# Kernel optimization log

Measured on AMD Instinct MI355X. Metric: run time of the kernel, lower is better.

Reference implementation:

```python
import jax, jax.numpy as jnp
import numpy as np
from jax import lax

B, L, N_NODES, N_SEQ = 256, 15360, 16, 64


def _lstm_layer(x, wih, whh, bih, bhh):
    # x: (B, T, I); torch gate order i, f, g, o
    H = whh.shape[1]
    b = bih + bhh
    def step(carry, xt):
        h, c = carry
        gates = xt @ wih.T + h @ whh.T + b
        i, f, g, o = jnp.split(gates, 4, axis=-1)
        c = jax.nn.sigmoid(f) * c + jax.nn.sigmoid(i) * jnp.tanh(g)
        h = jax.nn.sigmoid(o) * jnp.tanh(c)
        return (h, c), h
    h0 = jnp.zeros((x.shape[0], H), x.dtype)
    _, ys = lax.scan(step, (h0, h0), x.transpose(1, 0, 2))
    return ys.transpose(1, 0, 2)


def setup_inputs() -> dict:
    ks = iter(jax.random.split(jax.random.key(0), 64))
    def rn(shape, scale=1.0):
        return (jax.random.normal(next(ks), shape) * scale).astype(jnp.float32)
    d = {"x": rn((B, 1, L))}
    chs = [1, 16, 32, 64]
    for i in range(3):
        cin, cout = chs[i], chs[i + 1]
        s = 1.0 / np.sqrt(cin * 5)
        d[f"cw{i}"] = rn((cout, cin, 5), s)
        d[f"cb{i}"] = rn((cout,), s)
        d[f"bng{i}"] = jnp.ones((cout,), jnp.float32)
        d[f"bnb{i}"] = jnp.zeros((cout,), jnp.float32)
        d[f"bnm{i}"] = jnp.zeros((cout,), jnp.float32)
        d[f"bnv{i}"] = jnp.ones((cout,), jnp.float32)
    Hh = 64
    for l in range(2):
        s = 1.0 / np.sqrt(Hh)
        d[f"wih{l}"] = rn((4 * Hh, 64), s)
        d[f"whh{l}"] = rn((4 * Hh, Hh), s)
        d[f"bih{l}"] = rn((4 * Hh,), s)
        d[f"bhh{l}"] = rn((4 * Hh,), s)
    gin = [256, 64, 64]
    for l in range(3):
        s = 1.0 / np.sqrt(gin[l])
        d[f"gw{l}"] = rn((64, gin[l]), s)
        d[f"gb{l}"] = rn((64,), s)
    d["clw"] = rn((5, 64), 0.125)
    d["clb"] = rn((5,), 0.125)
    return d


def reference(x, cw0, cb0, bng0, bnb0, bnm0, bnv0, cw1, cb1, bng1, bnb1, bnm1, bnv1, cw2, cb2, bng2, bnb2, bnm2, bnv2, wih0, whh0, bih0, bhh0, wih1, whh1, bih1, bhh1, gw0, gb0, gw1, gb1, gw2, gb2, clw, clb):
    h = x
    # CNN: [Conv1d(k=5,p=2) -> BN(eval) -> ReLU -> MaxPool(2)] x 3
    for cw, cb, g, b, m, v in ((cw0, cb0, bng0, bnb0, bnm0, bnv0),
                               (cw1, cb1, bng1, bnb1, bnm1, bnv1),
                               (cw2, cb2, bng2, bnb2, bnm2, bnv2)):
        h = lax.conv_general_dilated(h, cw, (1,), [(2, 2)], dimension_numbers=("NCH", "OIH", "NCH")) + cb[None, :, None]
        h = g[None, :, None] * (h - m[None, :, None]) * lax.rsqrt(v[None, :, None] + 1e-5) + b[None, :, None]
        h = jax.nn.relu(h)
        Bq, Cq, Lq = h.shape
        h = h.reshape(Bq, Cq, Lq // 2, 2).max(-1)
    # AdaptiveAvgPool1d(64): length divisible by 64 -> exact mean bins
    Bq, Cq, Lq = h.shape
    h = h.reshape(Bq, Cq, N_SEQ, Lq // N_SEQ).mean(-1)
    h = h.transpose(0, 2, 1)  # (B, 64, 64) = (batch, seq, channels)
    # 2-layer LSTM (dropout is identity in eval)
    h = _lstm_layer(h, wih0, whh0, bih0, bhh0)
    h = _lstm_layer(h, wih1, whh1, bih1, bhh1)
    # Graph builder: Pearson-style correlation + value thresholding
    Hf = h.reshape(Bq, -1)
    fpn = Hf.shape[1] // N_NODES  # 256 features per node
    nf = Hf[:, :N_NODES * fpn].reshape(Bq, N_NODES, fpn)
    cen = nf - nf.mean(-1, keepdims=True)
    nrm = cen / (jnp.std(cen, axis=-1, ddof=1, keepdims=True) + 1e-8)
    C = jnp.einsum("bnf,bmf->bnm", nrm, nrm) / fpn  # (B, N, N)
    Cf = C.reshape(Bq, -1)
    k = min(max(1, int((100.0 - 25.0) / 100.0 * Cf.shape[1])), Cf.shape[1] - 1)
    thr = jnp.sort(Cf, axis=1)[:, k - 1]  # torch.kthvalue(k)
    eye = jnp.eye(N_NODES, dtype=C.dtype)
    adj = (C > thr[:, None, None]).astype(C.dtype) * (1.0 - eye)
    # GCN: x = ReLU(W (x + A x) + b), 3 layers, then max over nodes
    g = nf
    for gw, gb in ((gw0, gb0), (gw1, gb1), (gw2, gb2)):
        g = jax.nn.relu((g + jnp.einsum("bnm,bmf->bnf", adj, g)) @ gw.T + gb)
    emb = g.max(axis=1)
    return emb @ clw.T + clb
```

## Files before the change

kernel.cpp:

```cpp
#include <hip/hip_runtime.h>
#include <math.h>

typedef __attribute__((ext_vector_type(2))) float v2f;

__global__ __launch_bounds__(256) void prep_weights_kernel(
    const float* __restrict__ cw0, const float* __restrict__ cb0,
    const float* __restrict__ bng0, const float* __restrict__ bnb0,
    const float* __restrict__ bnm0, const float* __restrict__ bnv0,
    const float* __restrict__ cw1, const float* __restrict__ cb1,
    const float* __restrict__ bng1, const float* __restrict__ bnb1,
    const float* __restrict__ bnm1, const float* __restrict__ bnv1,
    const float* __restrict__ cw2, const float* __restrict__ cb2,
    const float* __restrict__ bng2, const float* __restrict__ bnb2,
    const float* __restrict__ bnm2, const float* __restrict__ bnv2,
    const float* __restrict__ wih0, const float* __restrict__ whh0,
    const float* __restrict__ wih1, const float* __restrict__ whh1,
    float* __restrict__ wt1, float* __restrict__ b1,
    float* __restrict__ wt2, float* __restrict__ b2,
    float* __restrict__ w0f, float* __restrict__ b0f,
    float* __restrict__ wih0c, float* __restrict__ whh0c,
    float* __restrict__ wih1c, float* __restrict__ whh1c)
{
    int g = blockIdx.x * 256 + threadIdx.x;
    const int GS = 64 * 256;
    for (int i = g; i < 2560; i += GS) {
        int co = i & 31, r = i >> 5, t = r % 5, ci = r / 5;
        float s = bng1[co] * rsqrtf(bnv1[co] + 1e-5f);
        wt1[i] = cw1[(co * 16 + ci) * 5 + t] * s;
    }
    if (g < 32) {
        float s = bng1[g] * rsqrtf(bnv1[g] + 1e-5f);
        b1[g] = (cb1[g] - bnm1[g]) * s + bnb1[g];
    }
    for (int i = g; i < 10240; i += GS) {
        int co = i & 63, r = i >> 6, t = r % 5, ci = r / 5;
        float s = bng2[co] * rsqrtf(bnv2[co] + 1e-5f);
        wt2[i] = cw2[(co * 32 + ci) * 5 + t] * s;
    }
    if (g < 64) {
        float s = bng2[g] * rsqrtf(bnv2[g] + 1e-5f);
        b2[g] = (cb2[g] - bnm2[g]) * s + bnb2[g];
    }
    if (g < 80) {
        int co = g / 5;
        float s = bng0[co] * rsqrtf(bnv0[co] + 1e-5f);
        w0f[g] = cw0[g] * s;
    }
    if (g < 16) {
        float s = bng0[g] * rsqrtf(bnv0[g] + 1e-5f);
        b0f[g] = (cb0[g] - bnm0[g]) * s + bnb0[g];
    }
    for (int i = g; i < 16384; i += GS) {
        int c = i & 3, r = (i >> 2) & 255, k4 = i >> 10;
        int src = r * 64 + k4 * 4 + c;
        wih0c[i] = wih0[src];
        whh0c[i] = whh0[src];
        wih1c[i] = wih1[src];
        whh1c[i] = whh1[src];
    }
}

__global__ __launch_bounds__(256) void convall_kernel(
    const float* __restrict__ x,
    const float* __restrict__ w0f, const float* __restrict__ b0f,
    const float* __restrict__ wt1, const float* __restrict__ b1,
    const float* __restrict__ wt2, const float* __restrict__ b2,
    const float* __restrict__ wih0c,
    const float* __restrict__ bih0, const float* __restrict__ bhh0,
    float* __restrict__ xg0g)
{
    __shared__ float U[8096];
    float* raw = &U[4064];
    int b = blockIdx.y, bx = blockIdx.x, tid = threadIdx.x;
    const float* xb = x + (size_t)b * 15360;
    {
        int base = 480 * bx - 14;
        for (int i = tid; i < 508; i += 256) {
            int g = base + i;
            raw[i] = (g >= 0 && g < 15360) ? xb[g] : 0.f;
        }
    }
    __syncthreads();
    {
        int ci0 = tid >> 4, sub = tid & 15;
        float w0 = w0f[ci0*5+0], w1 = w0f[ci0*5+1], w2 = w0f[ci0*5+2],
              w3 = w0f[ci0*5+3], w4 = w0f[ci0*5+4];
        float bb = b0f[ci0];
        int r0g = 240 * bx - 6;
        for (int p = sub; p < 252; p += 16) {
            int r = r0g + p;
            float v = 0.f;
            if (r >= 0 && r < 7680) {
                int i0 = 2 * p;
                float c0 = raw[i0],   c1 = raw[i0+1], c2 = raw[i0+2],
                      c3 = raw[i0+3], c4 = raw[i0+4], c5 = raw[i0+5];
                float s0 = fmaf(w0,c0, fmaf(w1,c1, fmaf(w2,c2, fmaf(w3,c3, w4*c4))));
                float s1 = fmaf(w0,c1, fmaf(w1,c2, fmaf(w2,c3, fmaf(w3,c4, w4*c5))));
                v = fmaxf(fmaxf(s0, s1) + bb, 0.f);
            }
            U[ci0 * 254 + p] = v;
        }
    }
    __syncthreads();
    {
        int cg = tid >> 7, jj = tid & 127;
        int cgu = __builtin_amdgcn_readfirstlane(cg);
        if (tid < 64) { int co = tid >> 1, c = 124 + (tid & 1); U[4064 + co * 126 + c] = 0.f; }
        if (jj < 124) {
            const float* wb = wt1 + cgu * 16;
            v2f a0[8], a1[8];
#pragma unroll
            for (int q = 0; q < 8; ++q) { a0[q] = (v2f){0.f,0.f}; a1[q] = (v2f){0.f,0.f}; }
#pragma unroll 4
            for (int ci = 0; ci < 16; ++ci) {
                const float2* xr = reinterpret_cast<const float2*>(&U[ci * 254]);
                float2 xA = xr[jj], xB = xr[jj + 1], xC = xr[jj + 2];
                float xv[6] = { xA.x, xA.y, xB.x, xB.y, xC.x, xC.y };
#pragma unroll
                for (int t = 0; t < 5; ++t) {
                    const v2f* wp2 = reinterpret_cast<const v2f*>(wb + (ci * 5 + t) * 32);
                    v2f va = { xv[t], xv[t] };
                    v2f vc = { xv[t + 1], xv[t + 1] };
#pragma unroll
                    for (int q2 = 0; q2 < 8; ++q2) {
                        v2f w = wp2[q2];
                        a0[q2] = __builtin_elementwise_fma(w, va, a0[q2]);
                        a1[q2] = __builtin_elementwise_fma(w, vc, a1[q2]);
                    }
                }
            }
            int q = 120 * bx - 2 + jj;
            bool ok = (q >= 0 && q < 3840);
#pragma unroll
            for (int q2 = 0; q2 < 8; ++q2) {
#pragma unroll
                for (int cpp = 0; cpp < 2; ++cpp) {
                    int qq = 2 * q2 + cpp;
                    int co = cgu * 16 + qq;
                    float val = 0.f;
                    if (ok) val = fmaxf(fmaxf(a0[q2][cpp], a1[q2][cpp]) + b1[co], 0.f);
                    U[4064 + co * 126 + jj] = val;
                }
            }
        }
    }
    __syncthreads();
    {
        int cg = tid >> 6, jj = tid & 63;
        int jje = (jj < 59) ? jj : 59;
        int cgu = __builtin_amdgcn_readfirstlane(cg);
        const float* wb = wt2 + cgu * 16;
        v2f a0[8], a1[8];
#pragma unroll
        for (int q = 0; q < 8; ++q) { a0[q] = (v2f){0.f,0.f}; a1[q] = (v2f){0.f,0.f}; }
#pragma unroll 4
        for (int ci = 0; ci < 32; ++ci) {
            const float2* xr = reinterpret_cast<const float2*>(&U[4064 + ci * 126]);
            float2 xA = xr[jje], xB = xr[jje + 1], xC = xr[jje + 2];
            float xv[6] = { xA.x, xA.y, xB.x, xB.y, xC.x, xC.y };
#pragma unroll
            for (int t = 0; t < 5; ++t) {
                const v2f* wp2 = reinterpret_cast<const v2f*>(wb + (ci * 5 + t) * 64);
                v2f va = { xv[t], xv[t] };
                v2f vc = { xv[t + 1], xv[t + 1] };
#pragma unroll
                for (int q2 = 0; q2 < 8; ++q2) {
                    v2f w = wp2[q2];
                    a0[q2] = __builtin_elementwise_fma(w, va, a0[q2]);
                    a1[q2] = __builtin_elementwise_fma(w, vc, a1[q2]);
                }
            }
        }
        __syncthreads();
        if (jj < 60) {
#pragma unroll
            for (int q2 = 0; q2 < 8; ++q2) {
#pragma unroll
                for (int cpp = 0; cpp < 2; ++cpp) {
                    int qq = 2 * q2 + cpp;
                    int co = cgu * 16 + qq;
                    float m = fmaxf(a0[q2][cpp], a1[q2][cpp]) + b2[co];
                    U[co * 61 + jj] = fmaxf(m, 0.f);
                }
            }
        }
    }
    __syncthreads();
    if (tid < 128) {
        int co = tid & 63, bin = tid >> 6;
        const float* r = U + co * 61 + bin * 30;
        float s = 0.f;
#pragma unroll
        for (int k = 0; k < 30; ++k) s += r[k];
        U[3904 + bin * 64 + co] = s * (1.f / 30.f);
    }
    __syncthreads();
    {
        int r = tid;
        float bias0 = bih0[r] + bhh0[r];
        float wr0[64];
#pragma unroll
        for (int k4 = 0; k4 < 16; ++k4) {
            float4 w4 = reinterpret_cast<const float4*>(wih0c)[k4 * 256 + r];
            wr0[k4*4+0] = w4.x; wr0[k4*4+1] = w4.y;
            wr0[k4*4+2] = w4.z; wr0[k4*4+3] = w4.w;
        }
#pragma unroll
        for (int bin = 0; bin < 2; ++bin) {
            float s0 = bias0, s1 = 0.f, s2 = 0.f, s3 = 0.f;
#pragma unroll
            for (int k4 = 0; k4 < 16; ++k4) {
                float4 xv4 = *reinterpret_cast<const float4*>(&U[3904 + bin * 64 + k4 * 4]);
                s0 = fmaf(wr0[k4*4+0], xv4.x, s0);
                s1 = fmaf(wr0[k4*4+1], xv4.y, s1);
                s2 = fmaf(wr0[k4*4+2], xv4.z, s2);
                s3 = fmaf(wr0[k4*4+3], xv4.w, s3);
            }
            xg0g[((size_t)b * 64 + 2 * bx + bin) * 256 + r] = (s0 + s1) + (s2 + s3);
        }
    }
}

__global__ __launch_bounds__(512) void lstmgraph_kernel(
    const float* __restrict__ xg0g, float* __restrict__ xg1g,
    const float* __restrict__ whh0c, const float* __restrict__ wih1c,
    const float* __restrict__ whh1c,
    const float* __restrict__ bih1, const float* __restrict__ bhh1,
    const float* __restrict__ gw0, const float* __restrict__ gb0,
    const float* __restrict__ gw1, const float* __restrict__ gb1,
    const float* __restrict__ gw2, const float* __restrict__ gb2,
    const float* __restrict__ clw, const float* __restrict__ clb,
    float* __restrict__ out)
{
    __shared__ float xb[64][64];
    __shared__ float G[12228];
    float* gbuf = G;
    float* hbw  = G + 512;
    int b = blockIdx.x;
    int tid = threadIdx.x;
    int wv = tid >> 6, ln = tid & 63;
    size_t base0 = (size_t)b * 16384;
    float wr[64];
    if (wv < 4) {
#pragma unroll
        for (int k4 = 0; k4 < 16; ++k4) {
            float4 w4 = reinterpret_cast<const float4*>(whh0c)[k4 * 256 + tid];
            wr[k4*4+0] = w4.x; wr[k4*4+1] = w4.y;
            wr[k4*4+2] = w4.z; wr[k4*4+3] = w4.w;
        }
        hbw[wv * 64 + ln] = 0.f;
    }
    float c = 0.f;
    float xg_cur = (wv < 4) ? xg0g[base0 + tid] : 0.f;
    for (int t = 0; t < 64; ++t) {
        float xg_nxt = 0.f;
        if (wv < 4 && t < 63) xg_nxt = xg0g[base0 + (size_t)(t + 1) * 256 + tid];
        if (wv < 4) {
            float s0 = xg_cur, s1 = 0.f, s2 = 0.f, s3 = 0.f;
#pragma unroll
            for (int k4 = 0; k4 < 16; ++k4) {
                float4 hv4 = *reinterpret_cast<const float4*>(&hbw[wv * 64 + k4 * 4]);
                s0 = fmaf(wr[k4*4+0], hv4.x, s0);
                s1 = fmaf(wr[k4*4+1], hv4.y, s1);
                s2 = fmaf(wr[k4*4+2], hv4.z, s2);
                s3 = fmaf(wr[k4*4+3], hv4.w, s3);
            }
            float acc = (s0 + s1) + (s2 + s3);
            float a;
            if (wv == 2) a = tanhf(acc);
            else         a = 1.f / (1.f + __expf(-acc));
            gbuf[(t & 1) * 256 + wv * 64 + ln] = a;
        }
        __syncthreads();
        if (wv < 4) {
            float gi = gbuf[(t & 1) * 256 + 0 * 64 + ln], gf = gbuf[(t & 1) * 256 + 1 * 64 + ln],
                  gg = gbuf[(t & 1) * 256 + 2 * 64 + ln], go = gbuf[(t & 1) * 256 + 3 * 64 + ln];
            c = fmaf(gf, c, gi * gg);
            float h = go * tanhf(c);
            hbw[wv * 64 + ln] = h;
            if (wv == 0) xb[t][ln] = h;
        }
        xg_cur = xg_nxt;
    }
    __syncthreads();
    {
        int r = tid & 255;
        int tb = (tid >> 8) * 32;
        float bias1 = bih1[r] + bhh1[r];
        float wr1[64];
#pragma unroll
        for (int k4 = 0; k4 < 16; ++k4) {
            float4 w4 = reinterpret_cast<const float4*>(wih1c)[k4 * 256 + r];
            wr1[k4*4+0] = w4.x; wr1[k4*4+1] = w4.y;
            wr1[k4*4+2] = w4.z; wr1[k4*4+3] = w4.w;
        }
        for (int tt = 0; tt < 32; ++tt) {
            int t = tb + tt;
            float s0 = bias1, s1 = 0.f, s2 = 0.f, s3 = 0.f;
#pragma unroll
            for (int k4 = 0; k4 < 16; ++k4) {
                float4 xv4 = *reinterpret_cast<const float4*>(&xb[t][k4 * 4]);
                s0 = fmaf(wr1[k4*4+0], xv4.x, s0);
                s1 = fmaf(wr1[k4*4+1], xv4.y, s1);
                s2 = fmaf(wr1[k4*4+2], xv4.z, s2);
                s3 = fmaf(wr1[k4*4+3], xv4.w, s3);
            }
            xg1g[base0 + (size_t)t * 256 + r] = (s0 + s1) + (s2 + s3);
        }
    }
    if (wv < 4) {
#pragma unroll
        for (int k4 = 0; k4 < 16; ++k4) {
            float4 w4 = reinterpret_cast<const float4*>(whh1c)[k4 * 256 + tid];
            wr[k4*4+0] = w4.x; wr[k4*4+1] = w4.y;
            wr[k4*4+2] = w4.z; wr[k4*4+3] = w4.w;
        }
        hbw[wv * 64 + ln] = 0.f;
    }
    c = 0.f;
    __syncthreads();
    xg_cur = (wv < 4) ? xg1g[base0 + tid] : 0.f;
    for (int t = 0; t < 64; ++t) {
        float xg_nxt = 0.f;
        if (wv < 4 && t < 63) xg_nxt = xg1g[base0 + (size_t)(t + 1) * 256 + tid];
        if (wv < 4) {
            float s0 = xg_cur, s1 = 0.f, s2 = 0.f, s3 = 0.f;
#pragma unroll
            for (int k4 = 0; k4 < 16; ++k4) {
                float4 hv4 = *reinterpret_cast<const float4*>(&hbw[wv * 64 + k4 * 4]);
                s0 = fmaf(wr[k4*4+0], hv4.x, s0);
                s1 = fmaf(wr[k4*4+1], hv4.y, s1);
                s2 = fmaf(wr[k4*4+2], hv4.z, s2);
                s3 = fmaf(wr[k4*4+3], hv4.w, s3);
            }
            float acc = (s0 + s1) + (s2 + s3);
            float a;
            if (wv == 2) a = tanhf(acc);
            else         a = 1.f / (1.f + __expf(-acc));
            gbuf[(t & 1) * 256 + wv * 64 + ln] = a;
        }
        __syncthreads();
        if (wv < 4) {
            float gi = gbuf[(t & 1) * 256 + 0 * 64 + ln], gf = gbuf[(t & 1) * 256 + 1 * 64 + ln],
                  gg = gbuf[(t & 1) * 256 + 2 * 64 + ln], go = gbuf[(t & 1) * 256 + 3 * 64 + ln];
            c = fmaf(gf, c, gi * gg);
            float h = go * tanhf(c);
            hbw[wv * 64 + ln] = h;
            if (wv == 0) xb[t][ln] = h;
        }
        xg_cur = xg_nxt;
    }
    __syncthreads();
    float* nf   = G;
    float* sb   = G + 4112;
    float* red  = G + 8224;
    float* mean = G + 8496;
    float* rstd = G + 8512;
    float* C    = G + 8528;
    float* adj  = G + 8784;
    float* thrv = G + 9040;
    float* bufA = G + 9044;
    float* bufB = G + 10084;
    float* bufC = G + 11124;
    float* emb  = G + 12164;
    for (int i = tid; i < 4096; i += 512) {
        int n = i >> 8, f = i & 255;
        nf[n * 257 + f] = xb[4 * n + (f >> 6)][f & 63];
    }
    __syncthreads();
    int nd = (tid >> 4) & 15, sub = tid & 15;
    if (tid < 256) {
        float s = 0.f;
        for (int f = sub; f < 256; f += 16) s += nf[nd * 257 + f];
        red[nd * 17 + sub] = s;
    }
    __syncthreads();
    if (tid < 16) {
        float m = 0.f;
        for (int i = 0; i < 16; ++i) m += red[tid * 17 + i];
        mean[tid] = m * (1.f / 256.f);
    }
    __syncthreads();
    if (tid < 256) {
        float mu = mean[nd];
        float ss = 0.f;
        for (int f = sub; f < 256; f += 16) { float d = nf[nd * 257 + f] - mu; ss = fmaf(d, d, ss); }
        red[nd * 17 + sub] = ss;
    }
    __syncthreads();
    if (tid < 16) {
        float m = 0.f;
        for (int i = 0; i < 16; ++i) m += red[tid * 17 + i];
        rstd[tid] = 1.f / (sqrtf(m * (1.f / 255.f)) + 1e-8f);
    }
    __syncthreads();
    for (int i = tid; i < 4096; i += 512) {
        int n = i >> 8, f = i & 255;
        sb[n * 257 + f] = (nf[n * 257 + f] - mean[n]) * rstd[n];
    }
    __syncthreads();
    if (tid < 256) {
        int n = tid >> 4, m = tid & 15;
        float a0 = 0, a1 = 0, a2 = 0, a3 = 0;
        for (int f = 0; f < 256; f += 4) {
            a0 = fmaf(sb[n * 257 + f + 0], sb[m * 257 + f + 0], a0);
            a1 = fmaf(sb[n * 257 + f + 1], sb[m * 257 + f + 1], a1);
            a2 = fmaf(sb[n * 257 + f + 2], sb[m * 257 + f + 2], a2);
            a3 = fmaf(sb[n * 257 + f + 3], sb[m * 257 + f + 3], a3);
        }
        C[tid] = ((a0 + a1) + (a2 + a3)) * (1.f / 256.f);
    }
    __syncthreads();
    if (tid < 256) {
        float v = C[tid];
        int cnt = 0, eq = 0;
        for (int j2 = 0; j2 < 256; ++j2) {
            float vj = C[j2];
            cnt += (vj < v);
            eq  += (vj == v);
        }
        if (cnt <= 191 && 191 < cnt + eq) thrv[0] = v;
    }
    __syncthreads();
    if (tid < 256) {
        int n = tid >> 4, m = tid & 15;
        adj[tid] = (C[tid] > thrv[0] && n != m) ? 1.f : 0.f;
    }
    __syncthreads();
    for (int i = tid; i < 4096; i += 512) {
        int n = i >> 8, f = i & 255;
        float acc = nf[n * 257 + f];
#pragma unroll
        for (int m = 0; m < 16; ++m) acc = fmaf(adj[n * 16 + m], nf[m * 257 + f], acc);
        sb[n * 257 + f] = acc;
    }
    __syncthreads();
    for (int i = tid; i < 1024; i += 512) {
        int n = i >> 6, o = i & 63;
        const float4* wr4 = reinterpret_cast<const float4*>(gw0 + (size_t)o * 256);
        float acc = gb0[o];
        for (int f4 = 0; f4 < 64; ++f4) {
            float4 wv4 = wr4[f4];
            int f = f4 * 4;
            acc = fmaf(sb[n * 257 + f + 0], wv4.x, acc);
            acc = fmaf(sb[n * 257 + f + 1], wv4.y, acc);
            acc = fmaf(sb[n * 257 + f + 2], wv4.z, acc);
            acc = fmaf(sb[n * 257 + f + 3], wv4.w, acc);
        }
        bufA[n * 65 + o] = fmaxf(acc, 0.f);
    }
    __syncthreads();
    for (int i = tid; i < 1024; i += 512) {
        int n = i >> 6, f = i & 63;
        float acc = bufA[n * 65 + f];
#pragma unroll
        for (int m = 0; m < 16; ++m) acc = fmaf(adj[n * 16 + m], bufA[m * 65 + f], acc);
        bufB[n * 65 + f] = acc;
    }
    __syncthreads();
    for (int i = tid; i < 1024; i += 512) {
        int n = i >> 6, o = i & 63;
        const float4* wr4 = reinterpret_cast<const float4*>(gw1 + (size_t)o * 64);
        float acc = gb1[o];
        for (int f4 = 0; f4 < 16; ++f4) {
            float4 wv4 = wr4[f4];
            int f = f4 * 4;
            acc = fmaf(bufB[n * 65 + f + 0], wv4.x, acc);
            acc = fmaf(bufB[n * 65 + f + 1], wv4.y, acc);
            acc = fmaf(bufB[n * 65 + f + 2], wv4.z, acc);
            acc = fmaf(bufB[n * 65 + f + 3], wv4.w, acc);
        }
        bufC[n * 65 + o] = fmaxf(acc, 0.f);
    }
    __syncthreads();
    for (int i = tid; i < 1024; i += 512) {
        int n = i >> 6, f = i & 63;
        float acc = bufC[n * 65 + f];
#pragma unroll
        for (int m = 0; m < 16; ++m) acc = fmaf(adj[n * 16 + m], bufC[m * 65 + f], acc);
        bufA[n * 65 + f] = acc;
    }
    __syncthreads();
    for (int i = tid; i < 1024; i += 512) {
        int n = i >> 6, o = i & 63;
        const float4* wr4 = reinterpret_cast<const float4*>(gw2 + (size_t)o * 64);
        float acc = gb2[o];
        for (int f4 = 0; f4 < 16; ++f4) {
            float4 wv4 = wr4[f4];
            int f = f4 * 4;
            acc = fmaf(bufA[n * 65 + f + 0], wv4.x, acc);
            acc = fmaf(bufA[n * 65 + f + 1], wv4.y, acc);
            acc = fmaf(bufA[n * 65 + f + 2], wv4.z, acc);
            acc = fmaf(bufA[n * 65 + f + 3], wv4.w, acc);
        }
        bufB[n * 65 + o] = fmaxf(acc, 0.f);
    }
    __syncthreads();
    if (tid < 64) {
        float mx = bufB[tid];
#pragma unroll
        for (int n = 1; n < 16; ++n) mx = fmaxf(mx, bufB[n * 65 + tid]);
        emb[tid] = mx;
    }
    __syncthreads();
    if (tid < 5) {
        float acc = clb[tid];
#pragma unroll
        for (int o = 0; o < 64; ++o) acc = fmaf(emb[o], clw[tid * 64 + o], acc);
        out[(size_t)b * 5 + tid] = acc;
    }
}

extern "C" void kernel_launch(void* const* d_in, const int* in_sizes, int n_in,
                              void* d_out, int out_size, void* d_ws, size_t ws_size,
                              hipStream_t stream)
{
    const float* x    = (const float*)d_in[0];
    const float* cw0  = (const float*)d_in[1];
    const float* cb0  = (const float*)d_in[2];
    const float* bng0 = (const float*)d_in[3];
    const float* bnb0 = (const float*)d_in[4];
    const float* bnm0 = (const float*)d_in[5];
    const float* bnv0 = (const float*)d_in[6];
    const float* cw1  = (const float*)d_in[7];
    const float* cb1  = (const float*)d_in[8];
    const float* bng1 = (const float*)d_in[9];
    const float* bnb1 = (const float*)d_in[10];
    const float* bnm1 = (const float*)d_in[11];
    const float* bnv1 = (const float*)d_in[12];
    const float* cw2  = (const float*)d_in[13];
    const float* cb2  = (const float*)d_in[14];
    const float* bng2 = (const float*)d_in[15];
    const float* bnb2 = (const float*)d_in[16];
    const float* bnm2 = (const float*)d_in[17];
    const float* bnv2 = (const float*)d_in[18];
    const float* wih0 = (const float*)d_in[19];
    const float* whh0 = (const float*)d_in[20];
    const float* bih0 = (const float*)d_in[21];
    const float* bhh0 = (const float*)d_in[22];
    const float* wih1 = (const float*)d_in[23];
    const float* whh1 = (const float*)d_in[24];
    const float* bih1 = (const float*)d_in[25];
    const float* bhh1 = (const float*)d_in[26];
    const float* gw0  = (const float*)d_in[27];
    const float* gb0  = (const float*)d_in[28];
    const float* gw1  = (const float*)d_in[29];
    const float* gb1  = (const float*)d_in[30];
    const float* gw2  = (const float*)d_in[31];
    const float* gb2  = (const float*)d_in[32];
    const float* clw  = (const float*)d_in[33];
    const float* clb  = (const float*)d_in[34];

    float* xg0   = (float*)d_ws;
    float* xg1   = xg0 + 4194304;
    float* wt1   = xg1 + 4194304;
    float* b1    = wt1 + 2560;
    float* wt2   = b1 + 32;
    float* b2    = wt2 + 10240;
    float* w0f   = b2 + 64;
    float* b0f   = w0f + 80;
    float* wih0c = b0f + 16;
    float* whh0c = wih0c + 16384;
    float* wih1c = whh0c + 16384;
    float* whh1c = wih1c + 16384;

    prep_weights_kernel<<<64, 256, 0, stream>>>(
        cw0, cb0, bng0, bnb0, bnm0, bnv0,
        cw1, cb1, bng1, bnb1, bnm1, bnv1,
        cw2, cb2, bng2, bnb2, bnm2, bnv2,
        wih0, whh0, wih1, whh1,
        wt1, b1, wt2, b2, w0f, b0f,
        wih0c, whh0c, wih1c, whh1c);
    convall_kernel<<<dim3(32, 256), 256, 0, stream>>>(
        x, w0f, b0f, wt1, b1, wt2, b2, wih0c, bih0, bhh0, xg0);
    lstmgraph_kernel<<<256, 512, 0, stream>>>(
        xg0, xg1, whh0c, wih1c, whh1c, bih1, bhh1,
        gw0, gb0, gw1, gb1, gw2, gb2, clw, clb, (float*)d_out);
}
```

Measured before the change: 462.4 us.

## Wavefront-pipeline both LSTM layers concurrently in one block, dropping xg1 buffer

The two LSTM layers now run concurrently across the 512 threads. Threads 0-255 run layer 0 at step s while threads 256-511 run layer 1 at step s-1, computing the input projection inline from the previous layer-0 output. The change removes the serial second recurrence, the separate xg1 projection pass and its global-memory round trip. Layer-1 threads do twice the FMAs per step and hold two 64-entry register weight arrays, which raises register pressure. Each step still takes two block barriers.

```diff
diff --git a/kernel.cpp b/kernel.cpp
--- a/kernel.cpp
+++ b/kernel.cpp
@@ -222,7 +222,7 @@
 }
 
 __global__ __launch_bounds__(512) void lstmgraph_kernel(
-    const float* __restrict__ xg0g, float* __restrict__ xg1g,
+    const float* __restrict__ xg0g,
     const float* __restrict__ whh0c, const float* __restrict__ wih1c,
     const float* __restrict__ whh1c,
     const float* __restrict__ bih1, const float* __restrict__ bhh1,
@@ -232,125 +232,123 @@
     const float* __restrict__ clw, const float* __restrict__ clb,
     float* __restrict__ out)
 {
-    __shared__ float xb[64][64];
-    __shared__ float G[12228];
-    float* gbuf = G;
-    float* hbw  = G + 512;
+    __shared__ float S[16384];
+    float* H1   = S;
+    float (*xb)[64] = (float(*)[64])(S + 4096);
+    float* gbufA = S + 8192;
+    float* gbufB = S + 8448;
+    float* hbwA  = S + 8704;
+    float* hbwB  = S + 8960;
     int b = blockIdx.x;
     int tid = threadIdx.x;
-    int wv = tid >> 6, ln = tid & 63;
+    int ln = tid & 63;
+    int gate = (tid >> 6) & 3;
+    bool inA = (tid < 256);
     size_t base0 = (size_t)b * 16384;
     float wr[64];
-    if (wv < 4) {
+    float wi[64];
+    float bias1 = 0.f;
+    if (inA) {
 #pragma unroll
         for (int k4 = 0; k4 < 16; ++k4) {
             float4 w4 = reinterpret_cast<const float4*>(whh0c)[k4 * 256 + tid];
             wr[k4*4+0] = w4.x; wr[k4*4+1] = w4.y;
             wr[k4*4+2] = w4.z; wr[k4*4+3] = w4.w;
         }
-        hbw[wv * 64 + ln] = 0.f;
-    }
-    float c = 0.f;
-    float xg_cur = (wv < 4) ? xg0g[base0 + tid] : 0.f;
-    for (int t = 0; t < 64; ++t) {
-        float xg_nxt = 0.f;
-        if (wv < 4 && t < 63) xg_nxt = xg0g[base0 + (size_t)(t + 1) * 256 + tid];
-        if (wv < 4) {
-            float s0 = xg_cur, s1 = 0.f, s2 = 0.f, s3 = 0.f;
-#pragma unroll
-            for (int k4 = 0; k4 < 16; ++k4) {
-                float4 hv4 = *reinterpret_cast<const float4*>(&hbw[wv * 64 + k4 * 4]);
-                s0 = fmaf(wr[k4*4+0], hv4.x, s0);
-                s1 = fmaf(wr[k4*4+1], hv4.y, s1);
-                s2 = fmaf(wr[k4*4+2], hv4.z, s2);
-                s3 = fmaf(wr[k4*4+3], hv4.w, s3);
-            }
-            float acc = (s0 + s1) + (s2 + s3);
-            float a;
-            if (wv == 2) a = tanhf(acc);
-            else         a = 1.f / (1.f + __expf(-acc));
-            gbuf[(t & 1) * 256 + wv * 64 + ln] = a;
-        }
-        __syncthreads();
-        if (wv < 4) {
-            float gi = gbuf[(t & 1) * 256 + 0 * 64 + ln], gf = gbuf[(t & 1) * 256 + 1 * 64 + ln],
-                  gg = gbuf[(t & 1) * 256 + 2 * 64 + ln], go = gbuf[(t & 1) * 256 + 3 * 64 + ln];
-            c = fmaf(gf, c, gi * gg);
-            float h = go * tanhf(c);
-            hbw[wv * 64 + ln] = h;
-            if (wv == 0) xb[t][ln] = h;
-        }
-        xg_cur = xg_nxt;
-    }
-    __syncthreads();
-    {
-        int r = tid & 255;
-        int tb = (tid >> 8) * 32;
-        float bias1 = bih1[r] + bhh1[r];
-        float wr1[64];
+        hbwA[tid] = 0.f;
+    } else {
+        int r = tid - 256;
 #pragma unroll
         for (int k4 = 0; k4 < 16; ++k4) {
-            float4 w4 = reinterpret_cast<const float4*>(wih1c)[k4 * 256 + r];
-            wr1[k4*4+0] = w4.x; wr1[k4*4+1] = w4.y;
-            wr1[k4*4+2] = w4.z; wr1[k4*4+3] = w4.w;
-        }
-        for (int tt = 0; tt < 32; ++tt) {
-            int t = tb + tt;
-            float s0 = bias1, s1 = 0.f, s2 = 0.f, s3 = 0.f;
-#pragma unroll
-            for (int k4 = 0; k4 < 16; ++k4) {
-                float4 xv4 = *reinterpret_cast<const float4*>(&xb[t][k4 * 4]);
-                s0 = fmaf(wr1[k4*4+0], xv4.x, s0);
-                s1 = fmaf(wr1[k4*4+1], xv4.y, s1);
-                s2 = fmaf(wr1[k4*4+2], xv4.z, s2);
-                s3 = fmaf(wr1[k4*4+3], xv4.w, s3);
-            }
-            xg1g[base0 + (size_t)t * 256 + r] = (s0 + s1) + (s2 + s3);
-        }
-    }
-    if (wv < 4) {
-#pragma unroll
-        for (int k4 = 0; k4 < 16; ++k4) {
-            float4 w4 = reinterpret_cast<const float4*>(whh1c)[k4 * 256 + tid];
+            float4 w4 = reinterpret_cast<const float4*>(whh1c)[k4 * 256 + r];
             wr[k4*4+0] = w4.x; wr[k4*4+1] = w4.y;
             wr[k4*4+2] = w4.z; wr[k4*4+3] = w4.w;
-        }
-        hbw[wv * 64 + ln] = 0.f;
-    }
-    c = 0.f;
-    __syncthreads();
-    xg_cur = (wv < 4) ? xg1g[base0 + tid] : 0.f;
-    for (int t = 0; t < 64; ++t) {
-        float xg_nxt = 0.f;
-        if (wv < 4 && t < 63) xg_nxt = xg1g[base0 + (size_t)(t + 1) * 256 + tid];
-        if (wv < 4) {
-            float s0 = xg_cur, s1 = 0.f, s2 = 0.f, s3 = 0.f;
-#pragma unroll
-            for (int k4 = 0; k4 < 16; ++k4) {
-                float4 hv4 = *reinterpret_cast<const float4*>(&hbw[wv * 64 + k4 * 4]);
-                s0 = fmaf(wr[k4*4+0], hv4.x, s0);
-                s1 = fmaf(wr[k4*4+1], hv4.y, s1);
-                s2 = fmaf(wr[k4*4+2], hv4.z, s2);
-                s3 = fmaf(wr[k4*4+3], hv4.w, s3);
-            }
-            float acc = (s0 + s1) + (s2 + s3);
-            float a;
-            if (wv == 2) a = tanhf(acc);
-            else         a = 1.f / (1.f + __expf(-acc));
-            gbuf[(t & 1) * 256 + wv * 64 + ln] = a;
+            float4 v4 = reinterpret_cast<const float4*>(wih1c)[k4 * 256 + r];
+            wi[k4*4+0] = v4.x; wi[k4*4+1] = v4.y;
+            wi[k4*4+2] = v4.z; wi[k4*4+3] = v4.w;
+        }
+        bias1 = bih1[r] + bhh1[r];
+        hbwB[r] = 0.f;
+    }
+    float c = 0.f;
+    float xgA = 0.f, xgN = 0.f;
+    if (inA) {
+        xgA = xg0g[base0 + tid];
+        xgN = xg0g[base0 + 256 + tid];
+    }
+    for (int s = 0; s <= 64; ++s) {
+        float xgP = 0.f;
+        float a = 0.f;
+        if (inA) {
+            if (s + 2 < 64) xgP = xg0g[base0 + (size_t)(s + 2) * 256 + tid];
+            if (s < 64) {
+                float s0 = xgA, s1 = 0.f, s2 = 0.f, s3 = 0.f;
+#pragma unroll
+                for (int k4 = 0; k4 < 16; ++k4) {
+                    float4 hv4 = *reinterpret_cast<const float4*>(&hbwA[gate * 0 + (tid >> 6) * 64 + k4 * 4]);
+                    s0 = fmaf(wr[k4*4+0], hv4.x, s0);
+                    s1 = fmaf(wr[k4*4+1], hv4.y, s1);
+                    s2 = fmaf(wr[k4*4+2], hv4.z, s2);
+                    s3 = fmaf(wr[k4*4+3], hv4.w, s3);
+                }
+                float acc = (s0 + s1) + (s2 + s3);
+                if (gate == 2) a = tanhf(acc);
+                else           a = 1.f / (1.f + __expf(-acc));
+                gbufA[tid] = a;
+            }
+        } else {
+            if (s >= 1) {
+                int t = s - 1;
+                float s0 = bias1, s1 = 0.f, s2 = 0.f, s3 = 0.f;
+#pragma unroll
+                for (int k4 = 0; k4 < 16; ++k4) {
+                    float4 xv4 = *reinterpret_cast<const float4*>(&xb[t][k4 * 4]);
+                    s0 = fmaf(wi[k4*4+0], xv4.x, s0);
+                    s1 = fmaf(wi[k4*4+1], xv4.y, s1);
+                    s2 = fmaf(wi[k4*4+2], xv4.z, s2);
+                    s3 = fmaf(wi[k4*4+3], xv4.w, s3);
+                }
+                float xg1 = (s0 + s1) + (s2 + s3);
+                s0 = xg1; s1 = 0.f; s2 = 0.f; s3 = 0.f;
+#pragma unroll
+                for (int k4 = 0; k4 < 16; ++k4) {
+                    float4 hv4 = *reinterpret_cast<const float4*>(&hbwB[gate * 64 + k4 * 4]);
+                    s0 = fmaf(wr[k4*4+0], hv4.x, s0);
+                    s1 = fmaf(wr[k4*4+1], hv4.y, s1);
+                    s2 = fmaf(wr[k4*4+2], hv4.z, s2);
+                    s3 = fmaf(wr[k4*4+3], hv4.w, s3);
+                }
+                float acc = (s0 + s1) + (s2 + s3);
+                if (gate == 2) a = tanhf(acc);
+                else           a = 1.f / (1.f + __expf(-acc));
+                gbufB[tid - 256] = a;
+            }
         }
         __syncthreads();
-        if (wv < 4) {
-            float gi = gbuf[(t & 1) * 256 + 0 * 64 + ln], gf = gbuf[(t & 1) * 256 + 1 * 64 + ln],
-                  gg = gbuf[(t & 1) * 256 + 2 * 64 + ln], go = gbuf[(t & 1) * 256 + 3 * 64 + ln];
-            c = fmaf(gf, c, gi * gg);
-            float h = go * tanhf(c);
-            hbw[wv * 64 + ln] = h;
-            if (wv == 0) xb[t][ln] = h;
-        }
-        xg_cur = xg_nxt;
-    }
-    __syncthreads();
+        if (inA) {
+            if (s < 64) {
+                float gi = gbufA[ln], gf = gbufA[64 + ln],
+                      gg = gbufA[128 + ln], go = gbufA[192 + ln];
+                c = fmaf(gf, c, gi * gg);
+                float h = go * tanhf(c);
+                hbwA[(tid >> 6) * 64 + ln] = h;
+                if (tid < 64) xb[s][ln] = h;
+            }
+        } else {
+            if (s >= 1) {
+                int t = s - 1;
+                float gi = gbufB[ln], gf = gbufB[64 + ln],
+                      gg = gbufB[128 + ln], go = gbufB[192 + ln];
+                c = fmaf(gf, c, gi * gg);
+                float h = go * tanhf(c);
+                hbwB[gate * 64 + ln] = h;
+                if (tid < 320) H1[t * 64 + ln] = h;
+            }
+        }
+        __syncthreads();
+        xgA = xgN; xgN = xgP;
+    }
+    float* G    = S + 4096;
     float* nf   = G;
     float* sb   = G + 4112;
     float* red  = G + 8224;
@@ -365,7 +363,7 @@
     float* emb  = G + 12164;
     for (int i = tid; i < 4096; i += 512) {
         int n = i >> 8, f = i & 255;
-        nf[n * 257 + f] = xb[4 * n + (f >> 6)][f & 63];
+        nf[n * 257 + f] = H1[(4 * n + (f >> 6)) * 64 + (f & 63)];
     }
     __syncthreads();
     int nd = (tid >> 4) & 15, sub = tid & 15;
@@ -552,8 +550,7 @@
     const float* clb  = (const float*)d_in[34];
 
     float* xg0   = (float*)d_ws;
-    float* xg1   = xg0 + 4194304;
-    float* wt1   = xg1 + 4194304;
+    float* wt1   = xg0 + 4194304;
     float* b1    = wt1 + 2560;
     float* wt2   = b1 + 32;
     float* b2    = wt2 + 10240;
@@ -574,6 +571,6 @@
     convall_kernel<<<dim3(32, 256), 256, 0, stream>>>(
         x, w0f, b0f, wt1, b1, wt2, b2, wih0c, bih0, bhh0, xg0);
     lstmgraph_kernel<<<256, 512, 0, stream>>>(
-        xg0, xg1, whh0c, wih1c, whh1c, bih1, bhh1,
+        xg0, whh0c, wih1c, whh1c, bih1, bhh1,
         gw0, gb0, gw1, gb1, gw2, gb2, clw, clb, (float*)d_out);
 }
```

After: 406.9 us. -12.0%, faster.
